# Performance work log

Hardware: AMD Instinct MI355X
Metric: run time of the kernel (lower is better)

The kernel has to match this reference:

```python
import jax, jax.numpy as jnp
import numpy as np

B, N, C = 32, 1025, 768
H, D = 12, 64          # num_heads, head_dim
M = 4 * D              # num random features = 256
HEIGHT, WIDTH = 32, 32 # spatial grid; N = HEIGHT*WIDTH + 1 (CLS)
EPS = 1e-6


def setup_inputs() -> dict:
    key = jax.random.key(0)
    ks = jax.random.split(key, 7)
    x = jax.random.normal(ks[0], (B, N, C), jnp.float32)
    w_qkv = jax.random.normal(ks[1], (3 * C, C), jnp.float32) * 0.02
    w_proj = jax.random.normal(ks[2], (C, C), jnp.float32) * 0.02
    b_proj = jnp.zeros((C,), jnp.float32)
    c_row = jax.random.normal(ks[3], (H, D), jnp.float32) * 0.02
    c_col = jax.random.normal(ks[4], (H, D), jnp.float32) * 0.02
    # orthogonal random-feature projection (m, d): QR blocks scaled by chi norm
    blocks = []
    for i in range(M // D):
        Hm = jax.random.normal(jax.random.fold_in(ks[5], i), (D, D), jnp.float32)
        Q, _ = jnp.linalg.qr(Hm)
        nrm = jnp.linalg.norm(jax.random.normal(jax.random.fold_in(ks[6], i), (D,), jnp.float32))
        blocks.append(Q * nrm)
    proj_feat = jnp.concatenate(blocks, axis=0)  # (M, D)
    return {"x": x, "w_qkv": w_qkv, "w_proj": w_proj, "b_proj": b_proj,
            "c_row": c_row, "c_col": c_col, "proj_feat": proj_feat}


def _string(xp, c_row, c_col):
    """Circulant-STRING rotation. xp: (B,H,Np,D)."""
    rows = jnp.arange(HEIGHT, dtype=jnp.float32)
    cols = jnp.arange(WIDTH, dtype=jnp.float32)
    gr, gc = jnp.meshgrid(rows, cols, indexing='ij')
    pos_r = gr.ravel()  # (Np,)
    pos_c = gc.ravel()
    # g: (H, Np, D)
    g = pos_r[None, :, None] * c_row[:, None, :] + pos_c[None, :, None] * c_col[:, None, :]
    g_fft = jnp.fft.fft(g, axis=-1)
    exp_lambda = jnp.exp(2j * g_fft.imag)          # (H, Np, D) complex, unit modulus
    x_fft = jnp.fft.fft(xp, axis=-1)               # (B, H, Np, D) complex
    rotated = jnp.fft.ifft(exp_lambda[None] * x_fft, axis=-1).real
    return rotated.astype(xp.dtype)


def _favor(x, proj):
    """Positive random feature map. x: (B,H,N,D), proj: (M,D) -> (B,H,N,M)."""
    xs = x * (D ** -0.25)
    px = jnp.einsum('bhnd,md->bhnm', xs, proj)
    norm_sq = 0.5 * jnp.sum(xs * xs, axis=-1, keepdims=True)
    return jnp.exp(px - norm_sq)


def reference(x, w_qkv, w_proj, b_proj, c_row, c_col, proj_feat):
    qkv = x @ w_qkv.T                                  # (B, N, 3C)
    qkv = qkv.reshape(B, N, 3, H, D).transpose(2, 0, 3, 1, 4)  # (3,B,H,N,D)
    q, k, v = qkv[0], qkv[1], qkv[2]
    # N == HEIGHT*WIDTH + 1 -> CLS token at position 0 is left unrotated
    q_cls, q_p = q[:, :, :1, :], q[:, :, 1:, :]
    k_cls, k_p = k[:, :, :1, :], k[:, :, 1:, :]
    q = jnp.concatenate([q_cls, _string(q_p, c_row, c_col)], axis=2)
    k = jnp.concatenate([k_cls, _string(k_p, c_row, c_col)], axis=2)
    q_feat = _favor(q, proj_feat)                      # (B,H,N,M)
    k_feat = _favor(k, proj_feat)
    # bidirectional linear attention
    context = jnp.einsum('bhnm,bhne->bhme', k_feat, v) # (B,H,M,D)
    num = jnp.einsum('bhnm,bhme->bhne', q_feat, context)
    k_sum = k_feat.sum(axis=2)                         # (B,H,M)
    den = jnp.einsum('bhnm,bhm->bhn', q_feat, k_sum)[..., None]
    den = jnp.maximum(den, EPS)
    out = num / den                                    # (B,H,N,D)
    out = out.transpose(0, 2, 1, 3).reshape(B, N, C)
    return out @ w_proj.T + b_proj
```

## Files before the change

### kernel.cpp

```cpp
#include <hip/hip_runtime.h>
#include <math.h>

typedef _Float16 f16;
typedef _Float16 f16x8 __attribute__((ext_vector_type(8)));
typedef _Float16 f16x4 __attribute__((ext_vector_type(4)));
typedef float f32x4 __attribute__((ext_vector_type(4)));

#define LDSK 40
#define NTOK 1025
#define CC 768
#define HH 12
#define DD 64
#define MM 256
#define VPAD 1056
#define BN_ROWS 32800

__device__ __forceinline__ void load_row16(const f16* p, f16x8& a0, f16x8& a1) {
    a0 = *(const f16x8*)p;
    a1 = *(const f16x8*)(p + 8);
}
__device__ __forceinline__ void load_row16(const float* p, f16x8& a0, f16x8& a1) {
    const float4* q = (const float4*)p;
    float4 u0 = q[0], u1 = q[1], u2 = q[2], u3 = q[3];
    a0[0] = (f16)u0.x; a0[1] = (f16)u0.y; a0[2] = (f16)u0.z; a0[3] = (f16)u0.w;
    a0[4] = (f16)u1.x; a0[5] = (f16)u1.y; a0[6] = (f16)u1.z; a0[7] = (f16)u1.w;
    a1[0] = (f16)u2.x; a1[1] = (f16)u2.y; a1[2] = (f16)u2.z; a1[3] = (f16)u2.w;
    a1[4] = (f16)u3.x; a1[5] = (f16)u3.y; a1[6] = (f16)u3.z; a1[7] = (f16)u3.w;
}

__device__ __forceinline__ void gload16(const f16* g, f16* l) {
    __builtin_amdgcn_global_load_lds(
        (const __attribute__((address_space(1))) unsigned int*)g,
        (__attribute__((address_space(3))) unsigned int*)l, 16, 0, 0);
}

__global__ void k_diag(float* out, float v) {
    if (threadIdx.x == 0 && blockIdx.x == 0) out[0] = v;
}

__global__ __launch_bounds__(256) void k_cvt_x(const float* __restrict__ x, f16* __restrict__ xw) {
    size_t i = ((size_t)blockIdx.x * 256 + threadIdx.x) * 4;
    float4 v;
    if (i < (size_t)BN_ROWS * CC) v = *(const float4*)(x + i);
    else v = make_float4(0.f, 0.f, 0.f, 0.f);
    f16x4 o; o[0] = (f16)v.x; o[1] = (f16)v.y; o[2] = (f16)v.z; o[3] = (f16)v.w;
    *(f16x4*)(xw + i) = o;
}

__global__ __launch_bounds__(256) void k_cvt(const float* __restrict__ in, f16* __restrict__ out,
                                             long n, float scale) {
    long i = (long)blockIdx.x * 256 + threadIdx.x;
    if (i < n) out[i] = (f16)(in[i] * scale);
}

__global__ __launch_bounds__(256) void k_zpad(f16* __restrict__ v16t) {
    int bh = blockIdx.x;
    for (int u = threadIdx.x; u < 64 * 31; u += 256) {
        int d = u / 31, j = u - d * 31;
        v16t[((size_t)bh * DD + d) * VPAD + 1025 + j] = (f16)0.f;
    }
}

__global__ __launch_bounds__(64) void k_ab(const float* __restrict__ c_row,
                                           const float* __restrict__ c_col,
                                           float* __restrict__ ab) {
    int h = blockIdx.x, k = threadIdx.x;
    float sa = 0.f, sb = 0.f;
    for (int d = 0; d < 64; ++d) {
        float s = sinf((float)((k * d) & 63) * (6.283185307179586f / 64.f));
        sa += c_row[h * 64 + d] * s;
        sb += c_col[h * 64 + d] * s;
    }
    ab[h * 64 + k] = -2.f * sa;
    ab[768 + h * 64 + k] = -2.f * sb;
}

__global__ __launch_bounds__(64) void k_wcirc(const float* __restrict__ ab, float* __restrict__ wc) {
    int hp = blockIdx.x; int h = hp >> 10; int p = hp & 1023;
    float pr = (float)(p >> 5), pc = (float)(p & 31);
    int t = threadIdx.x;
    __shared__ float th[64];
    th[t] = pr * ab[h * 64 + t] + pc * ab[768 + h * 64 + t];
    __syncthreads();
    float s = 0.f;
    #pragma unroll 8
    for (int k = 0; k < 64; ++k) {
        float arg = th[k] + (float)((k * t) & 63) * (6.283185307179586f / 64.f);
        s += __cosf(arg);
    }
    wc[(size_t)hp * 64 + t] = s * (1.f / 64.f);
}

template <bool GA, typename TA, typename TB>
__device__ __forceinline__ void gemm128_core(const TA* __restrict__ A, const TB* __restrict__ Bm,
                                             int K, int row0, int col0, int Alim,
                                             f32x4 (&acc)[4][4],
                                             f16 (*As)[LDSK], f16 (*Bs)[LDSK]) {
    const int tid = threadIdx.x;
    const int lane = tid & 63;
    const int lr = tid >> 1, lk = (tid & 1) * 16;
    const int frow = lane & 15, fk = (lane >> 4) * 8;
    const int wave = tid >> 6, wr = wave >> 1, wc = wave & 1;
    for (int kt = 0; kt < K; kt += 32) {
        f16x8 a0 = {}, a1 = {}, b0, b1;
        if (!GA || (row0 + lr) < Alim)
            load_row16(A + (size_t)(row0 + lr) * K + kt + lk, a0, a1);
        load_row16(Bm + (size_t)(col0 + lr) * K + kt + lk, b0, b1);
        __syncthreads();
        *(f16x8*)&As[lr][lk] = a0; *(f16x8*)&As[lr][lk + 8] = a1;
        *(f16x8*)&Bs[lr][lk] = b0; *(f16x8*)&Bs[lr][lk + 8] = b1;
        __syncthreads();
        f16x8 af[4], bf[4];
        #pragma unroll
        for (int m = 0; m < 4; ++m) af[m] = *(const f16x8*)&As[wr * 64 + m * 16 + frow][fk];
        #pragma unroll
        for (int n = 0; n < 4; ++n) bf[n] = *(const f16x8*)&Bs[wc * 64 + n * 16 + frow][fk];
        #pragma unroll
        for (int m = 0; m < 4; ++m)
            #pragma unroll
            for (int n = 0; n < 4; ++n)
                acc[m][n] = __builtin_amdgcn_mfma_f32_16x16x32_f16(af[m], bf[n], acc[m][n], 0, 0, 0);
    }
}

__device__ __forceinline__ void gemm128_dma(const f16* __restrict__ A, const f16* __restrict__ Bm,
                                            int K, int row0, int col0,
                                            f32x4 (&acc)[4][4], f16* As, f16* Bs) {
    const int tid = threadIdx.x;
    const int lane = tid & 63, wave = tid >> 6;
    const int frow = lane & 15, fk8 = (lane >> 4) * 8;
    const int wr = wave >> 1, wc = wave & 1;
    const int srow = lane >> 2;
    const int scol = (lane & 3) * 8;
    const f16* aG = A + (size_t)(row0 + wave * 32 + srow) * K + scol;
    const f16* bG = Bm + (size_t)(col0 + wave * 32 + srow) * K + scol;
    const size_t rstep = (size_t)16 * K;
    f16* aL0 = As + (wave * 32) * 32;
    f16* aL1 = As + (wave * 32 + 16) * 32;
    f16* bL0 = Bs + (wave * 32) * 32;
    f16* bL1 = Bs + (wave * 32 + 16) * 32;
    for (int kt = 0; kt < K; kt += 32) {
        __syncthreads();
        gload16(aG + kt, aL0);
        gload16(aG + kt + rstep, aL1);
        gload16(bG + kt, bL0);
        gload16(bG + kt + rstep, bL1);
        __syncthreads();
        f16x8 af[4], bf[4];
        #pragma unroll
        for (int m = 0; m < 4; ++m) af[m] = *(const f16x8*)&As[(wr * 64 + m * 16 + frow) * 32 + fk8];
        #pragma unroll
        for (int n = 0; n < 4; ++n) bf[n] = *(const f16x8*)&Bs[(wc * 64 + n * 16 + frow) * 32 + fk8];
        #pragma unroll
        for (int m = 0; m < 4; ++m)
            #pragma unroll
            for (int n = 0; n < 4; ++n)
                acc[m][n] = __builtin_amdgcn_mfma_f32_16x16x32_f16(af[m], bf[n], acc[m][n], 0, 0, 0);
    }
}

__device__ __forceinline__ void qkv_epilogue(f32x4 (&acc)[4][4], int row0, int col0,
                                             f16* __restrict__ q16, f16* __restrict__ k16,
                                             f16* __restrict__ v16t) {
    int lane = threadIdx.x & 63, wave = threadIdx.x >> 6;
    int wr = wave >> 1, wc = wave & 1;
    int rb = row0 + wr * 64 + 4 * (lane >> 4);
    int cb = col0 + wc * 64 + (lane & 15);
    #pragma unroll
    for (int m = 0; m < 4; ++m)
        #pragma unroll
        for (int n = 0; n < 4; ++n)
            #pragma unroll
            for (int i = 0; i < 4; ++i) {
                int r = rb + m * 16 + i;
                if (r >= BN_ROWS) continue;
                int j = cb + n * 16;
                int b = r / NTOK, nn = r - b * NTOK;
                int t = j / CC, rem = j - t * CC;
                int h = rem >> 6, d = rem & 63;
                size_t bh = (size_t)b * HH + h;
                f16 val = (f16)acc[m][n][i];
                if (t == 0) q16[(bh * NTOK + nn) * DD + d] = val;
                else if (t == 1) k16[(bh * NTOK + nn) * DD + d] = val;
                else v16t[(bh * DD + d) * VPAD + nn] = val;
            }
}

__global__ __launch_bounds__(256) void k_gemm_qkv_dma(const f16* __restrict__ A, const f16* __restrict__ Bm,
                                                      f16* __restrict__ q16, f16* __restrict__ k16,
                                                      f16* __restrict__ v16t) {
    __shared__ __attribute__((aligned(16))) f16 As[128 * 32];
    __shared__ __attribute__((aligned(16))) f16 Bs[128 * 32];
    const int q = 578, r = 2;
    int xg = blockIdx.x & 7, o8 = blockIdx.x >> 3;
    int wg = (xg < r ? xg * (q + 1) : r * (q + 1) + (xg - r) * q) + o8;
    int row0 = (wg / 18) * 128, col0 = (wg % 18) * 128;
    f32x4 acc[4][4] = {};
    gemm128_dma(A, Bm, CC, row0, col0, acc, As, Bs);
    qkv_epilogue(acc, row0, col0, q16, k16, v16t);
}

__global__ __launch_bounds__(256) void k_gemm_qkv_f32(const float* __restrict__ A, const f16* __restrict__ Bm,
                                                      f16* __restrict__ q16, f16* __restrict__ k16,
                                                      f16* __restrict__ v16t) {
    __shared__ __attribute__((aligned(16))) f16 As[128][LDSK];
    __shared__ __attribute__((aligned(16))) f16 Bs[128][LDSK];
    f32x4 acc[4][4] = {};
    int row0 = blockIdx.x * 128, col0 = blockIdx.y * 128;
    gemm128_core<true>(A, Bm, CC, row0, col0, BN_ROWS, acc, As, Bs);
    qkv_epilogue(acc, row0, col0, q16, k16, v16t);
}

__global__ __launch_bounds__(256) void k_rotate(const float* __restrict__ wcirc,
                                                f16* __restrict__ q16, f16* __restrict__ k16,
                                                float* __restrict__ nsqq, float* __restrict__ nsqk) {
    const int p = blockIdx.x, h = blockIdx.y;
    const int nn = p + 1;
    const int tid = threadIdx.x;
    __shared__ float wl[64];
    __shared__ __attribute__((aligned(16))) f16 Ws[64][72];
    __shared__ __attribute__((aligned(16))) f16 Xs[64][72];
    if (tid < 64) wl[tid] = wcirc[((size_t)h * 1024 + p) * 64 + tid];
    {
        const int row = tid >> 2;
        const int ch = (tid & 3) * 16;
        const int b = row & 31;
        const f16* src = ((row < 32) ? q16 : k16) + (((size_t)b * HH + h) * NTOK + nn) * DD + ch;
        f16x8 v0 = *(const f16x8*)src;
        f16x8 v1 = *(const f16x8*)(src + 8);
        *(f16x8*)&Xs[row][ch] = v0;
        *(f16x8*)&Xs[row][ch + 8] = v1;
    }
    __syncthreads();
    #pragma unroll
    for (int j = 0; j < 16; ++j) {
        int idx = tid * 16 + j;
        int d = idx >> 6, m = idx & 63;
        Ws[d][m] = (f16)wl[(d - m) & 63];
    }
    __syncthreads();
    const int lane = tid & 63, wave = tid >> 6;
    const int frow = lane & 15, fk = (lane >> 4) * 8;
    f32x4 acc[4] = {};
    #pragma unroll
    for (int kt = 0; kt < 64; kt += 32) {
        f16x8 a = *(const f16x8*)&Xs[wave * 16 + frow][kt + fk];
        #pragma unroll
        for (int n = 0; n < 4; ++n) {
            f16x8 bfr = *(const f16x8*)&Ws[n * 16 + frow][kt + fk];
            acc[n] = __builtin_amdgcn_mfma_f32_16x16x32_f16(a, bfr, acc[n], 0, 0, 0);
        }
    }
    #pragma unroll
    for (int i = 0; i < 4; ++i) {
        int row = wave * 16 + 4 * (lane >> 4) + i;
        int b = row & 31;
        f16* dst = ((row < 32) ? q16 : k16) + (((size_t)b * HH + h) * NTOK + nn) * DD;
        float ss = 0.f;
        #pragma unroll
        for (int n = 0; n < 4; ++n) {
            float v = acc[n][i];
            dst[n * 16 + (lane & 15)] = (f16)v;
            ss += v * v;
        }
        ss += __shfl_xor(ss, 1); ss += __shfl_xor(ss, 2);
        ss += __shfl_xor(ss, 4); ss += __shfl_xor(ss, 8);
        if ((lane & 15) == 0) {
            float* nd = (row < 32) ? nsqq : nsqk;
            nd[((size_t)b * HH + h) * NTOK + nn] = ss * (1.f / 16.f);
        }
    }
}

__global__ __launch_bounds__(256) void k_cls_nsq(const f16* __restrict__ q16, const f16* __restrict__ k16,
                                                 float* __restrict__ nsqq, float* __restrict__ nsqk) {
    int gw = (blockIdx.x * 256 + threadIdx.x) >> 6;
    int lane = threadIdx.x & 63;
    int which = gw & 1; int bh = gw >> 1;
    const f16* src = (which ? k16 : q16) + (size_t)bh * NTOK * DD;
    float v = (float)src[lane];
    float ss = v * v;
    for (int off = 1; off < 64; off <<= 1) ss += __shfl_xor(ss, off);
    if (lane == 0) (which ? nsqk : nsqq)[(size_t)bh * NTOK] = ss * (1.f / 16.f);
}

__global__ __launch_bounds__(512) void k_fctx(const f16* __restrict__ k16, const f16* __restrict__ v16t,
                                              const f16* __restrict__ pfeat, const float* __restrict__ nsqk,
                                              f16* __restrict__ ctxT) {
    __shared__ __attribute__((aligned(16))) f16 uLDS[80 * 136];
    f16 (*fts)[LDSK] = (f16(*)[LDSK])uLDS;
    f16 (*cx)[136]   = (f16(*)[136])uLDS;
    const int bh = blockIdx.x;
    const int tid = threadIdx.x;
    const int lane = tid & 63, w = tid >> 6;
    const int frow = lane & 15, fk8 = (lane >> 4) * 8;
    const int m0 = w * 32;
    f16x8 pf[2][2];
    #pragma unroll
    for (int mf = 0; mf < 2; ++mf)
        #pragma unroll
        for (int kf = 0; kf < 2; ++kf)
            pf[mf][kf] = *(const f16x8*)&pfeat[(m0 + mf * 16 + frow) * DD + kf * 32 + fk8];
    const f16* kb_base = k16 + (size_t)bh * NTOK * DD;
    const f16* vb_base = v16t + (size_t)bh * DD * VPAD;
    const float* ns_base = nsqk + (size_t)bh * NTOK;
    f32x4 acc[2][5] = {};
    for (int n0 = 0; n0 < VPAD; n0 += 32) {
        f16x8 kb[2][2];
        #pragma unroll
        for (int nf = 0; nf < 2; ++nf) {
            int n = n0 + nf * 16 + frow;
            #pragma unroll
            for (int kf = 0; kf < 2; ++kf) {
                f16x8 z = {};
                if (n < NTOK) z = *(const f16x8*)&kb_base[(size_t)n * DD + kf * 32 + fk8];
                kb[nf][kf] = z;
            }
        }
        f32x4 fa[2][2] = {};
        #pragma unroll
        for (int kf = 0; kf < 2; ++kf)
            #pragma unroll
            for (int mf = 0; mf < 2; ++mf)
                #pragma unroll
                for (int nf = 0; nf < 2; ++nf)
                    fa[mf][nf] = __builtin_amdgcn_mfma_f32_16x16x32_f16(pf[mf][kf], kb[nf][kf], fa[mf][nf], 0, 0, 0);
        #pragma unroll
        for (int nf = 0; nf < 2; ++nf) {
            int ncol = n0 + nf * 16 + frow;
            float ns = (ncol < NTOK) ? ns_base[ncol] : 0.f;
            #pragma unroll
            for (int mf = 0; mf < 2; ++mf)
                #pragma unroll
                for (int i = 0; i < 4; ++i) {
                    int mloc = m0 + mf * 16 + 4 * (lane >> 4) + i;
                    float v = (ncol < NTOK) ? fminf(__expf(fa[mf][nf][i] - ns), 60000.f) : 0.f;
                    fts[mloc][nf * 16 + frow] = (f16)v;
                }
        }
        __syncthreads();
        f16x8 afr[2];
        #pragma unroll
        for (int mf = 0; mf < 2; ++mf) afr[mf] = *(const f16x8*)&fts[m0 + mf * 16 + frow][fk8];
        #pragma unroll
        for (int ef = 0; ef < 4; ++ef) {
            f16x8 bfr = *(const f16x8*)&vb_base[(size_t)(ef * 16 + frow) * VPAD + n0 + fk8];
            #pragma unroll
            for (int mf = 0; mf < 2; ++mf)
                acc[mf][ef] = __builtin_amdgcn_mfma_f32_16x16x32_f16(afr[mf], bfr, acc[mf][ef], 0, 0, 0);
        }
        {
            f16x8 bfr;
            #pragma unroll
            for (int j = 0; j < 8; ++j)
                bfr[j] = (f16)((frow == 0 && (n0 + fk8 + j) < NTOK) ? 1.f : 0.f);
            #pragma unroll
            for (int mf = 0; mf < 2; ++mf)
                acc[mf][4] = __builtin_amdgcn_mfma_f32_16x16x32_f16(afr[mf], bfr, acc[mf][4], 0, 0, 0);
        }
        __syncthreads();
    }
    #pragma unroll
    for (int p = 0; p < 2; ++p) {
        __syncthreads();
        if ((w >> 2) == p) {
            int mb = m0 - p * 128;
            #pragma unroll
            for (int mf = 0; mf < 2; ++mf)
                #pragma unroll
                for (int ef = 0; ef < 5; ++ef) {
                    int e = ef * 16 + frow;
                    f16x4 pk;
                    #pragma unroll
                    for (int i = 0; i < 4; ++i) pk[i] = (f16)acc[mf][ef][i];
                    *(f16x4*)&cx[e][mb + mf * 16 + 4 * (lane >> 4)] = pk;
                }
        }
        __syncthreads();
        for (int u = tid; u < 80 * 16; u += 512) {
            int e = u >> 4, seg = u & 15;
            *(f16x8*)&ctxT[((size_t)bh * 80 + e) * MM + p * 128 + seg * 8] =
                *(const f16x8*)&cx[e][seg * 8];
        }
    }
}

__global__ __launch_bounds__(256) void k_fnum(const f16* __restrict__ q16, const f16* __restrict__ pfeat,
                                              const float* __restrict__ nsqq, const f16* __restrict__ ctxT,
                                              f16* __restrict__ attn) {
    __shared__ __attribute__((aligned(16))) f16 qf_s[128][72];
    const int bh = blockIdx.y;
    const int b = bh / HH, h = bh - b * HH;
    const int t0 = blockIdx.x * 128;
    const int tid = threadIdx.x;
    const int lane = tid & 63, w = tid >> 6;
    const int frow = lane & 15, fk8 = (lane >> 4) * 8;
    const f16* qbase = q16 + (size_t)bh * NTOK * DD;
    const f16* cbase = ctxT + (size_t)bh * 80 * MM;
    f16x8 qa[2][2];
    float ns[2][4];
    #pragma unroll
    for (int tf = 0; tf < 2; ++tf) {
        int t = t0 + w * 32 + tf * 16 + frow;
        #pragma unroll
        for (int kf = 0; kf < 2; ++kf) {
            f16x8 z = {};
            if (t < NTOK) z = *(const f16x8*)&qbase[(size_t)t * DD + kf * 32 + fk8];
            qa[tf][kf] = z;
        }
        #pragma unroll
        for (int i = 0; i < 4; ++i) {
            int tr = t0 + w * 32 + tf * 16 + 4 * (lane >> 4) + i;
            ns[tf][i] = (tr < NTOK) ? nsqq[(size_t)bh * NTOK + tr] : 0.f;
        }
    }
    f32x4 acc[2][5] = {};
    #pragma unroll
    for (int mc = 0; mc < 8; ++mc) {
        f16x8 pb[2][2];
        #pragma unroll
        for (int nf = 0; nf < 2; ++nf)
            #pragma unroll
            for (int kf = 0; kf < 2; ++kf)
                pb[nf][kf] = *(const f16x8*)&pfeat[(mc * 32 + nf * 16 + frow) * DD + kf * 32 + fk8];
        f32x4 fa[2][2] = {};
        #pragma unroll
        for (int kf = 0; kf < 2; ++kf)
            #pragma unroll
            for (int tf = 0; tf < 2; ++tf)
                #pragma unroll
                for (int nf = 0; nf < 2; ++nf)
                    fa[tf][nf] = __builtin_amdgcn_mfma_f32_16x16x32_f16(qa[tf][kf], pb[nf][kf], fa[tf][nf], 0, 0, 0);
        #pragma unroll
        for (int tf = 0; tf < 2; ++tf)
            #pragma unroll
            for (int nf = 0; nf < 2; ++nf)
                #pragma unroll
                for (int i = 0; i < 4; ++i) {
                    int tl = w * 32 + tf * 16 + 4 * (lane >> 4) + i;
                    float v = fminf(__expf(fa[tf][nf][i] - ns[tf][i]), 60000.f);
                    qf_s[tl][nf * 16 + frow] = (f16)v;
                }
        __syncthreads();
        f16x8 afr[2];
        #pragma unroll
        for (int tf = 0; tf < 2; ++tf) afr[tf] = *(const f16x8*)&qf_s[w * 32 + tf * 16 + frow][fk8];
        #pragma unroll
        for (int ef = 0; ef < 5; ++ef) {
            f16x8 bfr = *(const f16x8*)&cbase[(size_t)(ef * 16 + frow) * MM + mc * 32 + fk8];
            #pragma unroll
            for (int tf = 0; tf < 2; ++tf)
                acc[tf][ef] = __builtin_amdgcn_mfma_f32_16x16x32_f16(afr[tf], bfr, acc[tf][ef], 0, 0, 0);
        }
        __syncthreads();
    }
    #pragma unroll
    for (int tf = 0; tf < 2; ++tf)
        #pragma unroll
        for (int i = 0; i < 4; ++i) {
            float den = fmaxf(__shfl(acc[tf][4][i], lane & 48), 1e-6f);
            int tl = w * 32 + tf * 16 + 4 * (lane >> 4) + i;
            #pragma unroll
            for (int ef = 0; ef < 4; ++ef)
                qf_s[tl][ef * 16 + frow] = (f16)(acc[tf][ef][i] / den);
        }
    __syncthreads();
    for (int u = tid; u < 128 * 8; u += 256) {
        int tok = u >> 3, seg = u & 7;
        if (t0 + tok < NTOK)
            *(f16x8*)&attn[((size_t)(b * NTOK + t0 + tok)) * CC + h * DD + seg * 8] =
                *(const f16x8*)&qf_s[tok][seg * 8];
    }
}

__device__ __forceinline__ void proj_epilogue(f32x4 (&acc)[4][4], int row0, int col0,
                                              const float* __restrict__ bias, float* __restrict__ out) {
    int lane = threadIdx.x & 63, wave = threadIdx.x >> 6;
    int wr = wave >> 1, wc = wave & 1;
    int rb = row0 + wr * 64 + 4 * (lane >> 4);
    int cb = col0 + wc * 64 + (lane & 15);
    #pragma unroll
    for (int n = 0; n < 4; ++n) {
        int j = cb + n * 16;
        float bj = bias[j];
        #pragma unroll
        for (int m = 0; m < 4; ++m)
            #pragma unroll
            for (int i = 0; i < 4; ++i) {
                int r = rb + m * 16 + i;
                if (r < BN_ROWS) out[(size_t)r * CC + j] = acc[m][n][i] + bj;
            }
    }
}

__global__ __launch_bounds__(256) void k_gemm_proj_dma(const f16* __restrict__ A, const f16* __restrict__ Bm,
                                                       const float* __restrict__ bias, float* __restrict__ out) {
    __shared__ __attribute__((aligned(16))) f16 As[128 * 32];
    __shared__ __attribute__((aligned(16))) f16 Bs[128 * 32];
    const int q = 192, r = 6;
    int xg = blockIdx.x & 7, o8 = blockIdx.x >> 3;
    int wg = (xg < r ? xg * (q + 1) : r * (q + 1) + (xg - r) * q) + o8;
    int row0 = (wg / 6) * 128, col0 = (wg % 6) * 128;
    f32x4 acc[4][4] = {};
    gemm128_dma(A, Bm, CC, row0, col0, acc, As, Bs);
    proj_epilogue(acc, row0, col0, bias, out);
}

__global__ __launch_bounds__(256) void k_gemm_proj(const f16* __restrict__ A, const f16* __restrict__ Bm,
                                                   const float* __restrict__ bias, float* __restrict__ out) {
    __shared__ __attribute__((aligned(16))) f16 As[128][LDSK];
    __shared__ __attribute__((aligned(16))) f16 Bs[128][LDSK];
    f32x4 acc[4][4] = {};
    int row0 = blockIdx.x * 128, col0 = blockIdx.y * 128;
    gemm128_core<true>(A, Bm, CC, row0, col0, BN_ROWS, acc, As, Bs);
    proj_epilogue(acc, row0, col0, bias, out);
}

extern "C" void kernel_launch(void* const* d_in, const int* in_sizes, int n_in,
                              void* d_out, int out_size, void* d_ws, size_t ws_size,
                              hipStream_t stream) {
    const float* x = (const float*)d_in[0];
    const float* w_qkv = (const float*)d_in[1];
    const float* w_proj = (const float*)d_in[2];
    const float* b_proj = (const float*)d_in[3];
    const float* c_row = (const float*)d_in[4];
    const float* c_col = (const float*)d_in[5];
    const float* proj_feat = (const float*)d_in[6];
    float* out = (float*)d_out;
    char* ws = (char*)d_ws;
    char* ob = (char*)d_out;

    const size_t O_WQKV  = 0;
    const size_t O_WPROJ = 3538944;
    const size_t O_Q16   = 4718592;
    const size_t O_K16   = 55099392;
    const size_t O_XW    = 105480192;
    const size_t NEED_B  = 105480192;
    const size_t NEED_A  = 156008448;
    if (ws_size < NEED_B) {
        k_diag<<<1, 64, 0, stream>>>(out, (float)((double)ws_size / 1048576.0));
        return;
    }
    const bool useA = (ws_size >= NEED_A);

    const size_t OD_V    = 0;
    const size_t OD_CTX  = 51904512;
    const size_t OD_WC   = 67633152;
    const size_t OD_NSQQ = 70778880;
    const size_t OD_NSQK = 72353280;
    const size_t OD_PF   = 73927680;
    const size_t OD_AB   = 73960448;

    f16* wqkv16  = (f16*)(ws + O_WQKV);
    f16* wproj16 = (f16*)(ws + O_WPROJ);
    f16* q16     = (f16*)(ws + O_Q16);
    f16* k16     = (f16*)(ws + O_K16);
    f16* xw16    = (f16*)(ws + O_XW);
    f16* v16t    = (f16*)(ob + OD_V);
    f16* ctxT    = (f16*)(ob + OD_CTX);
    float* wcirc = (float*)(ob + OD_WC);
    float* nsqq  = (float*)(ob + OD_NSQQ);
    float* nsqk  = (float*)(ob + OD_NSQK);
    f16* pfeat16 = (f16*)(ob + OD_PF);
    float* ab    = (float*)(ob + OD_AB);
    f16* attn16  = k16;

    k_cvt<<<6912, 256, 0, stream>>>(w_qkv, wqkv16, 1769472L, 1.f);
    k_cvt<<<2304, 256, 0, stream>>>(w_proj, wproj16, 589824L, 1.f);
    k_cvt<<<64, 256, 0, stream>>>(proj_feat, pfeat16, 16384L, 0.3535533906f);
    k_ab<<<12, 64, 0, stream>>>(c_row, c_col, ab);
    k_wcirc<<<12288, 64, 0, stream>>>(ab, wcirc);

    if (useA) {
        k_cvt_x<<<24672, 256, 0, stream>>>(x, xw16);
        k_gemm_qkv_dma<<<4626, 256, 0, stream>>>(xw16, wqkv16, q16, k16, v16t);
    } else {
        k_gemm_qkv_f32<<<dim3(257, 18), 256, 0, stream>>>(x, wqkv16, q16, k16, v16t);
    }
    k_zpad<<<384, 256, 0, stream>>>(v16t);

    k_rotate<<<dim3(1024, 12), 256, 0, stream>>>(wcirc, q16, k16, nsqq, nsqk);
    k_cls_nsq<<<192, 256, 0, stream>>>(q16, k16, nsqq, nsqk);

    k_fctx<<<384, 512, 0, stream>>>(k16, v16t, pfeat16, nsqk, ctxT);
    k_fnum<<<dim3(9, 384), 256, 0, stream>>>(q16, pfeat16, nsqq, ctxT, attn16);

    if (useA) {
        k_gemm_proj_dma<<<1542, 256, 0, stream>>>(attn16, wproj16, b_proj, out);
    } else {
        k_gemm_proj<<<dim3(257, 6), 256, 0, stream>>>(attn16, wproj16, b_proj, out);
    }

    (void)in_sizes; (void)n_in; (void)out_size;
}
```

Before: 669.7 us.

## Double K-tile depth with XOR-swizzled LDS and software-prefetch operands in attention kernels

The DMA GEMM used for the QKV and output projections now stages 64-wide K tiles, so it runs half as many barrier pairs per tile. The LDS rows are XOR-swizzled, and the MFMA fragment reads apply the matching swizzle to avoid bank conflicts. The context kernel issues the V fragment loads early and prefetches the next K tile into registers while the current one is computed. The output kernel prefetches the next random-feature projection block the same way. In exchange, LDS use per GEMM block doubles and register pressure rises, which may lower occupancy.

```diff
diff --git a/kernel.cpp b/kernel.cpp
--- a/kernel.cpp
+++ b/kernel.cpp
@@ -130,32 +130,36 @@
     const int lane = tid & 63, wave = tid >> 6;
     const int frow = lane & 15, fk8 = (lane >> 4) * 8;
     const int wr = wave >> 1, wc = wave & 1;
-    const int srow = lane >> 2;
-    const int scol = (lane & 3) * 8;
+    const int srow = lane >> 3;
+    const int scol = ((lane & 7) ^ srow) * 8;
     const f16* aG = A + (size_t)(row0 + wave * 32 + srow) * K + scol;
     const f16* bG = Bm + (size_t)(col0 + wave * 32 + srow) * K + scol;
-    const size_t rstep = (size_t)16 * K;
-    f16* aL0 = As + (wave * 32) * 32;
-    f16* aL1 = As + (wave * 32 + 16) * 32;
-    f16* bL0 = Bs + (wave * 32) * 32;
-    f16* bL1 = Bs + (wave * 32 + 16) * 32;
-    for (int kt = 0; kt < K; kt += 32) {
-        __syncthreads();
-        gload16(aG + kt, aL0);
-        gload16(aG + kt + rstep, aL1);
-        gload16(bG + kt, bL0);
-        gload16(bG + kt + rstep, bL1);
-        __syncthreads();
-        f16x8 af[4], bf[4];
-        #pragma unroll
-        for (int m = 0; m < 4; ++m) af[m] = *(const f16x8*)&As[(wr * 64 + m * 16 + frow) * 32 + fk8];
-        #pragma unroll
-        for (int n = 0; n < 4; ++n) bf[n] = *(const f16x8*)&Bs[(wc * 64 + n * 16 + frow) * 32 + fk8];
-        #pragma unroll
-        for (int m = 0; m < 4; ++m)
+    f16* aL = As + (wave * 32) * 64;
+    f16* bL = Bs + (wave * 32) * 64;
+    const int cswz = (frow & 7) * 8;
+    for (int kt = 0; kt < K; kt += 64) {
+        __syncthreads();
+        #pragma unroll
+        for (int j = 0; j < 4; ++j) {
+            gload16(aG + kt + (size_t)(8 * j) * K, aL + (8 * j) * 64);
+            gload16(bG + kt + (size_t)(8 * j) * K, bL + (8 * j) * 64);
+        }
+        __syncthreads();
+        #pragma unroll
+        for (int ks = 0; ks < 2; ++ks) {
+            f16x8 af[4], bf[4];
+            #pragma unroll
+            for (int m = 0; m < 4; ++m)
+                af[m] = *(const f16x8*)&As[(wr * 64 + m * 16 + frow) * 64 + ((ks * 32 + fk8) ^ cswz)];
             #pragma unroll
             for (int n = 0; n < 4; ++n)
-                acc[m][n] = __builtin_amdgcn_mfma_f32_16x16x32_f16(af[m], bf[n], acc[m][n], 0, 0, 0);
+                bf[n] = *(const f16x8*)&Bs[(wc * 64 + n * 16 + frow) * 64 + ((ks * 32 + fk8) ^ cswz)];
+            #pragma unroll
+            for (int m = 0; m < 4; ++m)
+                #pragma unroll
+                for (int n = 0; n < 4; ++n)
+                    acc[m][n] = __builtin_amdgcn_mfma_f32_16x16x32_f16(af[m], bf[n], acc[m][n], 0, 0, 0);
+        }
     }
 }
 
@@ -189,8 +193,8 @@
 __global__ __launch_bounds__(256) void k_gemm_qkv_dma(const f16* __restrict__ A, const f16* __restrict__ Bm,
                                                       f16* __restrict__ q16, f16* __restrict__ k16,
                                                       f16* __restrict__ v16t) {
-    __shared__ __attribute__((aligned(16))) f16 As[128 * 32];
-    __shared__ __attribute__((aligned(16))) f16 Bs[128 * 32];
+    __shared__ __attribute__((aligned(16))) f16 As[128 * 64];
+    __shared__ __attribute__((aligned(16))) f16 Bs[128 * 64];
     const int q = 578, r = 2;
     int xg = blockIdx.x & 7, o8 = blockIdx.x >> 3;
     int wg = (xg < r ? xg * (q + 1) : r * (q + 1) + (xg - r) * q) + o8;
@@ -304,9 +308,7 @@
     const f16* kb_base = k16 + (size_t)bh * NTOK * DD;
     const f16* vb_base = v16t + (size_t)bh * DD * VPAD;
     const float* ns_base = nsqk + (size_t)bh * NTOK;
-    f32x4 acc[2][5] = {};
-    for (int n0 = 0; n0 < VPAD; n0 += 32) {
-        f16x8 kb[2][2];
+    auto loadK = [&](f16x8 (&kb)[2][2], int n0) {
         #pragma unroll
         for (int nf = 0; nf < 2; ++nf) {
             int n = n0 + nf * 16 + frow;
@@ -317,6 +319,15 @@
                 kb[nf][kf] = z;
             }
         }
+    };
+    f32x4 acc[2][5] = {};
+    f16x8 kb[2][2];
+    loadK(kb, 0);
+    for (int n0 = 0; n0 < VPAD; n0 += 32) {
+        f16x8 vb[4];
+        #pragma unroll
+        for (int ef = 0; ef < 4; ++ef)
+            vb[ef] = *(const f16x8*)&vb_base[(size_t)(ef * 16 + frow) * VPAD + n0 + fk8];
         f32x4 fa[2][2] = {};
         #pragma unroll
         for (int kf = 0; kf < 2; ++kf)
@@ -325,6 +336,8 @@
                 #pragma unroll
                 for (int nf = 0; nf < 2; ++nf)
                     fa[mf][nf] = __builtin_amdgcn_mfma_f32_16x16x32_f16(pf[mf][kf], kb[nf][kf], fa[mf][nf], 0, 0, 0);
+        f16x8 kbn[2][2];
+        loadK(kbn, n0 + 32);
         #pragma unroll
         for (int nf = 0; nf < 2; ++nf) {
             int ncol = n0 + nf * 16 + frow;
@@ -343,12 +356,10 @@
         #pragma unroll
         for (int mf = 0; mf < 2; ++mf) afr[mf] = *(const f16x8*)&fts[m0 + mf * 16 + frow][fk8];
         #pragma unroll
-        for (int ef = 0; ef < 4; ++ef) {
-            f16x8 bfr = *(const f16x8*)&vb_base[(size_t)(ef * 16 + frow) * VPAD + n0 + fk8];
+        for (int ef = 0; ef < 4; ++ef)
             #pragma unroll
             for (int mf = 0; mf < 2; ++mf)
-                acc[mf][ef] = __builtin_amdgcn_mfma_f32_16x16x32_f16(afr[mf], bfr, acc[mf][ef], 0, 0, 0);
-        }
+                acc[mf][ef] = __builtin_amdgcn_mfma_f32_16x16x32_f16(afr[mf], vb[ef], acc[mf][ef], 0, 0, 0);
         {
             f16x8 bfr;
             #pragma unroll
@@ -359,6 +370,11 @@
                 acc[mf][4] = __builtin_amdgcn_mfma_f32_16x16x32_f16(afr[mf], bfr, acc[mf][4], 0, 0, 0);
         }
         __syncthreads();
+        #pragma unroll
+        for (int nf = 0; nf < 2; ++nf)
+            #pragma unroll
+            for (int kf = 0; kf < 2; ++kf)
+                kb[nf][kf] = kbn[nf][kf];
     }
     #pragma unroll
     for (int p = 0; p < 2; ++p) {
@@ -414,15 +430,18 @@
             ns[tf][i] = (tr < NTOK) ? nsqq[(size_t)bh * NTOK + tr] : 0.f;
         }
     }
-    f32x4 acc[2][5] = {};
-    #pragma unroll
-    for (int mc = 0; mc < 8; ++mc) {
-        f16x8 pb[2][2];
+    auto loadPB = [&](f16x8 (&pb)[2][2], int mc) {
         #pragma unroll
         for (int nf = 0; nf < 2; ++nf)
             #pragma unroll
             for (int kf = 0; kf < 2; ++kf)
                 pb[nf][kf] = *(const f16x8*)&pfeat[(mc * 32 + nf * 16 + frow) * DD + kf * 32 + fk8];
+    };
+    f32x4 acc[2][5] = {};
+    f16x8 pb[2][2];
+    loadPB(pb, 0);
+    #pragma unroll
+    for (int mc = 0; mc < 8; ++mc) {
         f32x4 fa[2][2] = {};
         #pragma unroll
         for (int kf = 0; kf < 2; ++kf)
@@ -431,6 +450,8 @@
                 #pragma unroll
                 for (int nf = 0; nf < 2; ++nf)
                     fa[tf][nf] = __builtin_amdgcn_mfma_f32_16x16x32_f16(qa[tf][kf], pb[nf][kf], fa[tf][nf], 0, 0, 0);
+        f16x8 pbn[2][2];
+        loadPB(pbn, (mc + 1) & 7);
         #pragma unroll
         for (int tf = 0; tf < 2; ++tf)
             #pragma unroll
@@ -453,6 +474,11 @@
                 acc[tf][ef] = __builtin_amdgcn_mfma_f32_16x16x32_f16(afr[tf], bfr, acc[tf][ef], 0, 0, 0);
         }
         __syncthreads();
+        #pragma unroll
+        for (int nf = 0; nf < 2; ++nf)
+            #pragma unroll
+            for (int kf = 0; kf < 2; ++kf)
+                pb[nf][kf] = pbn[nf][kf];
     }
     #pragma unroll
     for (int tf = 0; tf < 2; ++tf)
@@ -495,8 +521,8 @@
 
 __global__ __launch_bounds__(256) void k_gemm_proj_dma(const f16* __restrict__ A, const f16* __restrict__ Bm,
                                                        const float* __restrict__ bias, float* __restrict__ out) {
-    __shared__ __attribute__((aligned(16))) f16 As[128 * 32];
-    __shared__ __attribute__((aligned(16))) f16 Bs[128 * 32];
+    __shared__ __attribute__((aligned(16))) f16 As[128 * 64];
+    __shared__ __attribute__((aligned(16))) f16 Bs[128 * 64];
     const int q = 192, r = 6;
     int xg = blockIdx.x & 7, o8 = blockIdx.x >> 3;
     int wg = (xg < r ? xg * (q + 1) : r * (q + 1) + (xg - r) * q) + o8;
```

After: 660.7 us. About the same (-1.4%).
